# Kernel tuning notes

Hardware: AMD Instinct MI355X
Metric: run time of the kernel (lower is better)

Reference implementation:

```python
import jax, jax.numpy as jnp
import numpy as np

N = 50000
E = 800000
IN_DIM = 256
HID = 64
HEADS = 4
OUT_DIM = 40
NEG_SLOPE = 0.2


def _gatv2_conv(x, src, dst, Wl, bl, Wr, br, att, bias, concat):
    """PyG GATv2Conv (share_weights=False, eval mode, no attn dropout).
    src -> message source nodes, dst -> target nodes (softmax over dst)."""
    H, C = att.shape
    n = x.shape[0]
    xl = (x @ Wl + bl).reshape(n, H, C)  # source/message transform (lin_l)
    xr = (x @ Wr + br).reshape(n, H, C)  # target transform (lin_r)
    # per-edge logits: [E, H]
    s = xl[src] + xr[dst]                                  # [E,H,C]
    e = jnp.einsum('ehc,hc->eh', jax.nn.leaky_relu(s, NEG_SLOPE), att)
    # segment softmax over incoming edges of each target node
    m = jax.ops.segment_max(e, dst, num_segments=n)        # [N,H]
    m = jnp.where(jnp.isfinite(m), m, 0.0)                 # empty segments
    ex = jnp.exp(e - m[dst])
    denom = jax.ops.segment_sum(ex, dst, num_segments=n)   # [N,H]
    alpha = ex / (denom[dst] + 1e-16)                      # [E,H]
    out = jax.ops.segment_sum(alpha[:, :, None] * xl[src], dst, num_segments=n)
    if concat:
        out = out.reshape(n, H * C)
    else:
        out = out.mean(axis=1)
    return out + bias


def setup_inputs() -> dict:
    key = jax.random.key(0)
    ks = jax.random.split(key, 12)
    sc = 0.05
    return {
        'x': jax.random.normal(ks[0], (N, IN_DIM), jnp.float32),
        'src': jax.random.randint(ks[1], (E,), 0, N, jnp.int32),
        'dst': jax.random.randint(ks[2], (E,), 0, N, jnp.int32),
        'Wl1': jax.random.normal(ks[3], (IN_DIM, HEADS * HID), jnp.float32) * sc,
        'bl1': jnp.zeros((HEADS * HID,), jnp.float32),
        'Wr1': jax.random.normal(ks[4], (IN_DIM, HEADS * HID), jnp.float32) * sc,
        'br1': jnp.zeros((HEADS * HID,), jnp.float32),
        'att1': jax.random.normal(ks[5], (HEADS, HID), jnp.float32) * sc,
        'bias1': jnp.zeros((HEADS * HID,), jnp.float32),
        'Wl2': jax.random.normal(ks[6], (HEADS * HID, HEADS * HID), jnp.float32) * sc,
        'bl2': jnp.zeros((HEADS * HID,), jnp.float32),
        'Wr2': jax.random.normal(ks[7], (HEADS * HID, HEADS * HID), jnp.float32) * sc,
        'br2': jnp.zeros((HEADS * HID,), jnp.float32),
        'att2': jax.random.normal(ks[8], (HEADS, HID), jnp.float32) * sc,
        'bias2': jnp.zeros((HID,), jnp.float32),
        'Wc': jax.random.normal(ks[9], (HID, OUT_DIM), jnp.float32) * sc,
        'bc': jnp.zeros((OUT_DIM,), jnp.float32),
    }


def reference(x, src, dst, Wl1, bl1, Wr1, br1, att1, bias1,
              Wl2, bl2, Wr2, br2, att2, bias2, Wc, bc):
    h = _gatv2_conv(x, src, dst, Wl1, bl1, Wr1, br1, att1, bias1, concat=True)
    h = jax.nn.relu(h)  # dropout p applied only in training; eval -> identity
    h = _gatv2_conv(h, src, dst, Wl2, bl2, Wr2, br2, att2, bias2, concat=False)
    h = jax.nn.relu(h)
    return h @ Wc + bc  # [N, OUT_DIM]
```

## Files before the change

kernel.cpp:

```cpp
#include <hip/hip_runtime.h>
#include <hip/hip_bf16.h>
#include <math.h>


#define IN_DIM 256
#define HIDHC 256
#define HID 64
#define OUT_DIM 40

using half8  = __attribute__((ext_vector_type(8))) _Float16;
using half4  = __attribute__((ext_vector_type(4))) _Float16;
using half2v = __attribute__((ext_vector_type(2))) _Float16;
using f32x4  = __attribute__((ext_vector_type(4))) float;

__device__ __forceinline__ void gload16(const void* g, void* l) {
    __builtin_amdgcn_global_load_lds(
        (const __attribute__((address_space(1))) void*)g,
        (__attribute__((address_space(3))) void*)l, 16, 0, 0);
}

__global__ void hist_csr_prep(const int* __restrict__ src, const int* __restrict__ dst,
                              int* __restrict__ deg, int* __restrict__ csr,
                              int* __restrict__ oflow_cnt, int* __restrict__ oflow,
                              int E, int nbh,
                              const float* __restrict__ x, _Float16* __restrict__ Af,
                              const float* __restrict__ W0, const float* __restrict__ W1,
                              const float* __restrict__ W2, const float* __restrict__ W3,
                              _Float16* __restrict__ T, int n4, int nb_cvt) {
    int bid = blockIdx.x;
    if (bid < nbh) {
        int i = bid * 256 + threadIdx.x;
        if (i < E) {
            int d = dst[i];
            int r = atomicAdd(&deg[d], 1);
            if (r < 64) {
                csr[d * 64 + r] = src[i];
            } else {
                int q = atomicAdd(oflow_cnt, 1);
                oflow[2 * q] = d;
                oflow[2 * q + 1] = src[i];
            }
        }
    } else if (bid < nbh + nb_cvt) {
        int i = (bid - nbh) * 256 + threadIdx.x;
        if (i >= n4) return;
        float4 v = ((const float4*)x)[i];
        half4 h = { (_Float16)v.x, (_Float16)v.y, (_Float16)v.z, (_Float16)v.w };
        int node = i >> 6;
        int kb = (i & 63) * 4;
        size_t a = (size_t)(node >> 7) * 32768 + (size_t)(kb >> 3) * 1024
                 + (size_t)(node & 127) * 8 + (kb & 7);
        *(half4*)(Af + a) = h;
    } else {
        int widx = bid - nbh - nb_cvt;
        int wsel = widx >> 8, k = widx & 255, nn = threadIdx.x;
        const float* Wsel = (wsel == 0) ? W0 : (wsel == 1) ? W1
                          : (wsel == 2) ? W2 : W3;
        float v = Wsel[k * 256 + nn];
        size_t a = (size_t)wsel * 65536
                 + (size_t)(nn >> 7) * 32768 + (size_t)(k >> 5) * 4096
                 + (size_t)((k >> 3) & 3) * 1024 + (size_t)(nn & 127) * 8 + (k & 7);
        T[a] = (_Float16)v;
    }
}


__device__ __forceinline__ void gemm_tile(
    const _Float16* __restrict__ Apk,
    const _Float16* __restrict__ W0, const float* __restrict__ b0, _Float16* __restrict__ C0,
    const _Float16* __restrict__ W1, const float* __restrict__ b1, _Float16* __restrict__ C1,
    int M, int bx, int by, _Float16* sA, _Float16* sW)
{
    int tid = threadIdx.x;
    int bm = bx * 128;
    int bn = by * 128;

    int lane = tid & 63, w = tid >> 6;
    int z  = w >> 2, wq = w & 3;
    int r = lane & 15, q = lane >> 4;
    int m0 = (wq >> 1) * 64, n0 = (wq & 1) * 64;

    const _Float16* Abase = Apk + (size_t)bx * 32768;
    const _Float16* W0b   = W0  + (size_t)by * 32768;
    const _Float16* W1b   = W1  + (size_t)by * 32768;
    int go = tid * 8;

    f32x4 acc[4][4];
    #pragma unroll
    for (int i = 0; i < 4; ++i)
        #pragma unroll
        for (int j = 0; j < 4; ++j) acc[i][j] = (f32x4)0.f;

    gload16(Abase + go, sA + go);
    gload16(W0b + go, sW + go);
    gload16(W1b + go, sW + 4096 + go);
    __builtin_amdgcn_s_waitcnt(0);
    __syncthreads();

    #pragma unroll 1
    for (int kt = 0; kt < 8; ++kt) {
        int buf = kt & 1;
        if (kt < 7) {
            int k0 = (kt + 1) * 4096;
            gload16(Abase + k0 + go, sA + (buf ^ 1) * 4096 + go);
            gload16(W0b + k0 + go, sW + ((buf ^ 1) * 2 + 0) * 4096 + go);
            gload16(W1b + k0 + go, sW + ((buf ^ 1) * 2 + 1) * 4096 + go);
        }
        half8 a[4], b[4];
        #pragma unroll
        for (int i = 0; i < 4; ++i) {
            a[i] = *(const half8*)(sA + buf * 4096 + (q * 128 + m0 + i * 16 + r) * 8);
            b[i] = *(const half8*)(sW + (buf * 2 + z) * 4096 + (q * 128 + n0 + i * 16 + r) * 8);
        }
        #pragma unroll
        for (int i = 0; i < 4; ++i)
            #pragma unroll
            for (int j = 0; j < 4; ++j)
                acc[i][j] = __builtin_amdgcn_mfma_f32_16x16x32_f16(a[i], b[j], acc[i][j], 0, 0, 0);
        __builtin_amdgcn_s_waitcnt(0);
        __syncthreads();
    }

    const float* bias = z ? b1 : b0;
    _Float16*    C    = z ? C1 : C0;

    float bv[4];
    #pragma unroll
    for (int j = 0; j < 4; ++j) bv[j] = bias[bn + n0 + j * 16 + r];
    #pragma unroll
    for (int i = 0; i < 4; ++i) {
        #pragma unroll
        for (int reg = 0; reg < 4; ++reg) {
            int orow = bm + m0 + i * 16 + q * 4 + reg;
            if (orow < M) {
                #pragma unroll
                for (int j = 0; j < 4; ++j)
                    C[(size_t)orow * 256 + bn + n0 + j * 16 + r] =
                        (_Float16)(acc[i][j][reg] + bv[j]);
            }
        }
    }
}

__global__ __launch_bounds__(512) void gemm_dual(
    const _Float16* __restrict__ Apk,
    const _Float16* __restrict__ W0, const float* __restrict__ b0, _Float16* __restrict__ C0,
    const _Float16* __restrict__ W1, const float* __restrict__ b1, _Float16* __restrict__ C1,
    int M)
{
    __shared__ __align__(16) _Float16 sA[2 * 4096];
    __shared__ __align__(16) _Float16 sW[2 * 2 * 4096];
    gemm_tile(Apk, W0, b0, C0, W1, b1, C1, M, blockIdx.x, blockIdx.y, sA, sW);
}


__global__ __launch_bounds__(256) void gat_node(
    const _Float16* __restrict__ xl, const _Float16* __restrict__ xr,
    const float* __restrict__ att, const float* __restrict__ bias,
    const int* __restrict__ degv, const int* __restrict__ csr_src,
    const int* __restrict__ oflow_cnt, const int* __restrict__ oflow,
    void* __restrict__ out0, int n, int mode)
{
    int wid = threadIdx.x >> 6;
    int node = (blockIdx.x << 2) + wid;
    if (node >= n) return;
    int lane = threadIdx.x & 63;
    int H = lane >> 5;
    int p = lane & 31;

    const half2v c02 = { (_Float16)0.2f, (_Float16)0.2f };

    half8 xrh = *(const half8*)(xr + (size_t)node * HIDHC + p * 8);
    half2v xr01 = __builtin_shufflevector(xrh, xrh, 0, 1);
    half2v xr23 = __builtin_shufflevector(xrh, xrh, 2, 3);
    half2v xr45 = __builtin_shufflevector(xrh, xrh, 4, 5);
    half2v xr67 = __builtin_shufflevector(xrh, xrh, 6, 7);

    float4 af0 = *(const float4*)(att + p * 8);
    float4 af1 = *(const float4*)(att + p * 8 + 4);
    half2v at01 = { (_Float16)af0.x, (_Float16)af0.y };
    half2v at23 = { (_Float16)af0.z, (_Float16)af0.w };
    half2v at45 = { (_Float16)af1.x, (_Float16)af1.y };
    half2v at67 = { (_Float16)af1.z, (_Float16)af1.w };

    float acc[8];
    #pragma unroll
    for (int k = 0; k < 8; ++k) acc[k] = 0.f;
    float d = 0.f;

    auto edge_compute = [&](half8 h) {
        half2v h01 = __builtin_shufflevector(h, h, 0, 1);
        half2v h23 = __builtin_shufflevector(h, h, 2, 3);
        half2v h45 = __builtin_shufflevector(h, h, 4, 5);
        half2v h67 = __builtin_shufflevector(h, h, 6, 7);
        half2v s01 = h01 + xr01, s23 = h23 + xr23, s45 = h45 + xr45, s67 = h67 + xr67;
        half2v l01 = __builtin_elementwise_max(s01, s01 * c02);
        half2v l23 = __builtin_elementwise_max(s23, s23 * c02);
        half2v l45 = __builtin_elementwise_max(s45, s45 * c02);
        half2v l67 = __builtin_elementwise_max(s67, s67 * c02);
        float e = __builtin_amdgcn_fdot2(l01, at01, 0.f, false);
        e = __builtin_amdgcn_fdot2(l23, at23, e, false);
        e = __builtin_amdgcn_fdot2(l45, at45, e, false);
        e = __builtin_amdgcn_fdot2(l67, at67, e, false);
        e += __shfl_xor(e, 1);
        e += __shfl_xor(e, 2);
        e += __shfl_xor(e, 4);
        float pw = __expf(e);
        d += pw;
        #pragma unroll
        for (int k = 0; k < 8; ++k) acc[k] = fmaf(pw, (float)h[k], acc[k]);
    };
    auto edge_compute_single = [&](half8 h) {
        half2v h01 = __builtin_shufflevector(h, h, 0, 1);
        half2v h23 = __builtin_shufflevector(h, h, 2, 3);
        half2v h45 = __builtin_shufflevector(h, h, 4, 5);
        half2v h67 = __builtin_shufflevector(h, h, 6, 7);
        half2v s01 = h01 + xr01, s23 = h23 + xr23, s45 = h45 + xr45, s67 = h67 + xr67;
        half2v l01 = __builtin_elementwise_max(s01, s01 * c02);
        half2v l23 = __builtin_elementwise_max(s23, s23 * c02);
        half2v l45 = __builtin_elementwise_max(s45, s45 * c02);
        half2v l67 = __builtin_elementwise_max(s67, s67 * c02);
        float e = __builtin_amdgcn_fdot2(l01, at01, 0.f, false);
        e = __builtin_amdgcn_fdot2(l23, at23, e, false);
        e = __builtin_amdgcn_fdot2(l45, at45, e, false);
        e = __builtin_amdgcn_fdot2(l67, at67, e, false);
        e += __shfl_xor(e, 1);
        e += __shfl_xor(e, 2);
        e += __shfl_xor(e, 4);
        float pw = (H == 0) ? __expf(e) : 0.f;
        d += pw;
        #pragma unroll
        for (int k = 0; k < 8; ++k) acc[k] = fmaf(pw, (float)h[k], acc[k]);
    };

    int dg = __builtin_amdgcn_readfirstlane(degv[node]);
    int j0 = node << 6;

    int fast = min(dg, 64);
    int npf = fast >> 1;
    int idxv = 0;
    if (lane < fast) idxv = csr_src[j0 + lane];

    half8 hA, hB;
    if (npf > 0) { int s = __shfl(idxv, 0 + H, 64); hA = *(const half8*)(xl + (size_t)s * HIDHC + p * 8); }
    if (npf > 1) { int s = __shfl(idxv, 2 + H, 64); hB = *(const half8*)(xl + (size_t)s * HIDHC + p * 8); }
    int t = 0;
    for (; t + 4 <= npf; t += 2) {
        half8 ha = hA, hb = hB;
        { int s = __shfl(idxv, (t + 2) * 2 + H, 64); hA = *(const half8*)(xl + (size_t)s * HIDHC + p * 8); }
        { int s = __shfl(idxv, (t + 3) * 2 + H, 64); hB = *(const half8*)(xl + (size_t)s * HIDHC + p * 8); }
        edge_compute(ha);
        edge_compute(hb);
    }
    if (t + 2 <= npf) {
        half8 ha = hA, hb = hB;
        if (t + 2 < npf) { int s = __shfl(idxv, (t + 2) * 2 + H, 64); hA = *(const half8*)(xl + (size_t)s * HIDHC + p * 8); }
        edge_compute(ha);
        edge_compute(hb);
        t += 2;
    }
    if (t < npf) {
        edge_compute(hA);
    }
    if (fast & 1) {
        int s0 = __shfl(idxv, fast - 1, 64);
        half8 h = *(const half8*)(xl + (size_t)s0 * HIDHC + p * 8);
        edge_compute_single(h);
    }

    if (dg > 64) {
        int cnt = __builtin_amdgcn_readfirstlane(oflow_cnt[0]);
        for (int k = 0; k < cnt; ++k) {
            int dd = __builtin_amdgcn_readfirstlane(oflow[2 * k]);
            if (dd == node) {
                int ss = __builtin_amdgcn_readfirstlane(oflow[2 * k + 1]);
                half8 h = *(const half8*)(xl + (size_t)ss * HIDHC + p * 8);
                edge_compute_single(h);
            }
        }
    }

    d += __shfl_xor(d, 32);
    #pragma unroll
    for (int k = 0; k < 8; ++k) acc[k] += __shfl_xor(acc[k], 32);

    float inv = 1.f / (d + 1e-16f);
    float o[8];
    #pragma unroll
    for (int k = 0; k < 8; ++k) o[k] = acc[k] * inv;

    if (mode == 0) {
        if (H == 0) {
            float4 b0 = *(const float4*)(bias + p * 8);
            float4 b1 = *(const float4*)(bias + p * 8 + 4);
            float bb[8] = { b0.x, b0.y, b0.z, b0.w, b1.x, b1.y, b1.z, b1.w };
            half8 hh;
            #pragma unroll
            for (int k = 0; k < 8; ++k) hh[k] = (_Float16)fmaxf(o[k] + bb[k], 0.f);
            _Float16* dstp = (_Float16*)out0 + (size_t)(node >> 7) * 32768
                           + (size_t)p * 1024 + (size_t)(node & 127) * 8;
            *(half8*)dstp = hh;
        }
    } else {
        #pragma unroll
        for (int k = 0; k < 8; ++k) {
            o[k] += __shfl_xor(o[k], 8);
            o[k] += __shfl_xor(o[k], 16);
        }
        if (lane < 8) {
            float4 b0 = *(const float4*)(bias + p * 8);
            float4 b1 = *(const float4*)(bias + p * 8 + 4);
            float bb[8] = { b0.x, b0.y, b0.z, b0.w, b1.x, b1.y, b1.z, b1.w };
            float4 o0, o1;
            o0.x = fmaxf(o[0] * 0.25f + bb[0], 0.f);
            o0.y = fmaxf(o[1] * 0.25f + bb[1], 0.f);
            o0.z = fmaxf(o[2] * 0.25f + bb[2], 0.f);
            o0.w = fmaxf(o[3] * 0.25f + bb[3], 0.f);
            o1.x = fmaxf(o[4] * 0.25f + bb[4], 0.f);
            o1.y = fmaxf(o[5] * 0.25f + bb[5], 0.f);
            o1.z = fmaxf(o[6] * 0.25f + bb[6], 0.f);
            o1.w = fmaxf(o[7] * 0.25f + bb[7], 0.f);
            float* dstp = (float*)out0 + (size_t)node * HID + p * 8;
            *(float4*)dstp = o0;
            *(float4*)(dstp + 4) = o1;
        }
    }
}


__global__ __launch_bounds__(256) void final_linear(
    const float* __restrict__ h2, const float* __restrict__ Wc,
    const float* __restrict__ bc, float* __restrict__ out, int n)
{
    __shared__ float Ws[HID * OUT_DIM];
    __shared__ float bs[OUT_DIM];
    __shared__ float hs[64][HID + 1];

    for (int i = threadIdx.x; i < HID * OUT_DIM; i += 256) Ws[i] = Wc[i];
    if (threadIdx.x < OUT_DIM) bs[threadIdx.x] = bc[threadIdx.x];

    int n0 = blockIdx.x * 64;
    for (int i = threadIdx.x; i < 64 * HID; i += 256) {
        int r = i >> 6, c = i & 63;
        int node = n0 + r;
        hs[r][c] = (node < n) ? h2[(size_t)node * HID + c] : 0.f;
    }
    __syncthreads();

    for (int idx = threadIdx.x; idx < 64 * OUT_DIM; idx += 256) {
        int r = idx / OUT_DIM, o = idx % OUT_DIM;
        int node = n0 + r;
        if (node < n) {
            float s = bs[o];
            #pragma unroll
            for (int c = 0; c < HID; ++c) s = fmaf(hs[r][c], Ws[c * OUT_DIM + o], s);
            out[(size_t)node * OUT_DIM + o] = s;
        }
    }
}


extern "C" void kernel_launch(void* const* d_in, const int* in_sizes, int n_in,
                              void* d_out, int out_size, void* d_ws, size_t ws_size,
                              hipStream_t stream) {
    const int N = in_sizes[0] / IN_DIM;
    const int E = in_sizes[1];

    const float* x    = (const float*)d_in[0];
    const int*   src  = (const int*)d_in[1];
    const int*   dst  = (const int*)d_in[2];
    const float* Wl1  = (const float*)d_in[3];
    const float* bl1  = (const float*)d_in[4];
    const float* Wr1  = (const float*)d_in[5];
    const float* br1  = (const float*)d_in[6];
    const float* att1 = (const float*)d_in[7];
    const float* bias1= (const float*)d_in[8];
    const float* Wl2  = (const float*)d_in[9];
    const float* bl2  = (const float*)d_in[10];
    const float* Wr2  = (const float*)d_in[11];
    const float* br2  = (const float*)d_in[12];
    const float* att2 = (const float*)d_in[13];
    const float* bias2= (const float*)d_in[14];
    const float* Wc   = (const float*)d_in[15];
    const float* bc   = (const float*)d_in[16];

    char* ws = (char*)d_ws;
    size_t off = 0;
    const int NT = (N + 127) / 128;
    _Float16* xlh = (_Float16*)(ws + off); off += (size_t)N * HIDHC * 2;
    _Float16* xrh = (_Float16*)(ws + off); off += (size_t)N * HIDHC * 2;
    _Float16* Af  = (_Float16*)(ws + off); off += (size_t)NT * 32768 * 2;
    float*    h2  = (float*)(ws + off);    off += (size_t)N * HID * 4;
    _Float16* Wt  = (_Float16*)(ws + off); off += (size_t)4 * 65536 * 2;
    int* deg      = (int*)(ws + off); off += (size_t)N * 4;
    int* oflow_cnt= (int*)(ws + off); off += 4;
    int* csr      = (int*)(ws + off); off += (size_t)N * 64 * 4;
    int* oflow    = (int*)(ws + off); off += (size_t)E * 2 * 4;

    hipMemsetAsync(deg, 0, ((size_t)N + 1) * 4, stream);
    if (N & 127)
        hipMemsetAsync(Af + (size_t)(NT - 1) * 32768, 0, 32768 * 2, stream);

    const int nbh = (E + 255) / 256;
    const int n4 = N * HIDHC / 4;
    const int nb_cvt = (n4 + 255) / 256;
    hist_csr_prep<<<nbh + nb_cvt + 1024, 256, 0, stream>>>(
        src, dst, deg, csr, oflow_cnt, oflow, E, nbh,
        x, Af, Wl1, Wr1, Wl2, Wr2, Wt, n4, nb_cvt);

    const int KW = 65536;
    gemm_dual<<<dim3(NT, 2), 512, 0, stream>>>(Af,
        Wt + 0 * KW, bl1, xlh,
        Wt + 1 * KW, br1, xrh, N);
    gat_node<<<(N + 3) / 4, 256, 0, stream>>>(xlh, xrh, att1, bias1, deg, csr,
                                              oflow_cnt, oflow, (void*)Af, N, 0);
    gemm_dual<<<dim3(NT, 2), 512, 0, stream>>>(Af,
        Wt + 2 * KW, bl2, xlh,
        Wt + 3 * KW, br2, xrh, N);
    gat_node<<<(N + 3) / 4, 256, 0, stream>>>(xlh, xrh, att2, bias2, deg, csr,
                                              oflow_cnt, oflow, (void*)h2, N, 1);
    final_linear<<<(N + 63) / 64, 256, 0, stream>>>(h2, Wc, bc, (float*)d_out, N);
}
```

Baseline: 386.0 us.

## Split CSR build into rank histogram and scatter fused with first GEMM

The first kernel now only computes each edge's rank within its destination via atomics and stores it. The scatter of source indices into the CSR slots (plus overflow handling) moves into a new kernel that also runs the first dual GEMM, with scatter blocks placed ahead of the GEMM tiles. The aim is to overlap the memory-bound scatter with compute-bound GEMM work and shorten the atomic-heavy prep kernel. In exchange it adds an E-sized rank array that must be written and then read back.

```diff
diff --git a/kernel.cpp b/kernel.cpp
--- a/kernel.cpp
+++ b/kernel.cpp
@@ -19,28 +19,16 @@
         (__attribute__((address_space(3))) void*)l, 16, 0, 0);
 }
 
-__global__ void hist_csr_prep(const int* __restrict__ src, const int* __restrict__ dst,
-                              int* __restrict__ deg, int* __restrict__ csr,
-                              int* __restrict__ oflow_cnt, int* __restrict__ oflow,
-                              int E, int nbh,
-                              const float* __restrict__ x, _Float16* __restrict__ Af,
-                              const float* __restrict__ W0, const float* __restrict__ W1,
-                              const float* __restrict__ W2, const float* __restrict__ W3,
-                              _Float16* __restrict__ T, int n4, int nb_cvt) {
+__global__ void hist_prep(const int* __restrict__ dst, int* __restrict__ deg,
+                          int* __restrict__ rank, int E, int nbh,
+                          const float* __restrict__ x, _Float16* __restrict__ Af,
+                          const float* __restrict__ W0, const float* __restrict__ W1,
+                          const float* __restrict__ W2, const float* __restrict__ W3,
+                          _Float16* __restrict__ T, int n4, int nb_cvt) {
     int bid = blockIdx.x;
     if (bid < nbh) {
         int i = bid * 256 + threadIdx.x;
-        if (i < E) {
-            int d = dst[i];
-            int r = atomicAdd(&deg[d], 1);
-            if (r < 64) {
-                csr[d * 64 + r] = src[i];
-            } else {
-                int q = atomicAdd(oflow_cnt, 1);
-                oflow[2 * q] = d;
-                oflow[2 * q + 1] = src[i];
-            }
-        }
+        if (i < E) rank[i] = atomicAdd(&deg[dst[i]], 1);
     } else if (bid < nbh + nb_cvt) {
         int i = (bid - nbh) * 256 + threadIdx.x;
         if (i >= n4) return;
@@ -151,6 +139,36 @@
     __shared__ __align__(16) _Float16 sA[2 * 4096];
     __shared__ __align__(16) _Float16 sW[2 * 2 * 4096];
     gemm_tile(Apk, W0, b0, C0, W1, b1, C1, M, blockIdx.x, blockIdx.y, sA, sW);
+}
+
+__global__ __launch_bounds__(512) void gemm_scatter(
+    const _Float16* __restrict__ Apk,
+    const _Float16* __restrict__ W0, const float* __restrict__ b0, _Float16* __restrict__ C0,
+    const _Float16* __restrict__ W1, const float* __restrict__ b1, _Float16* __restrict__ C1,
+    int M, int nbs,
+    const int* __restrict__ src, const int* __restrict__ dst,
+    const int* __restrict__ rank, int* __restrict__ csr,
+    int* __restrict__ oflow_cnt, int* __restrict__ oflow, int E)
+{
+    __shared__ __align__(16) _Float16 sA[2 * 4096];
+    __shared__ __align__(16) _Float16 sW[2 * 2 * 4096];
+    if ((int)blockIdx.x < nbs) {
+        int e = blockIdx.x * 512 + threadIdx.x;
+        if (e < E) {
+            int r = rank[e];
+            int d = dst[e];
+            if (r < 64) {
+                csr[d * 64 + r] = src[e];
+            } else {
+                int q = atomicAdd(oflow_cnt, 1);
+                oflow[2 * q] = d;
+                oflow[2 * q + 1] = src[e];
+            }
+        }
+        return;
+    }
+    int g = blockIdx.x - nbs;
+    gemm_tile(Apk, W0, b0, C0, W1, b1, C1, M, g >> 1, g & 1, sA, sW);
 }
 
 
@@ -394,6 +412,7 @@
     _Float16* Wt  = (_Float16*)(ws + off); off += (size_t)4 * 65536 * 2;
     int* deg      = (int*)(ws + off); off += (size_t)N * 4;
     int* oflow_cnt= (int*)(ws + off); off += 4;
+    int* rank     = (int*)(ws + off); off += (size_t)E * 4;
     int* csr      = (int*)(ws + off); off += (size_t)N * 64 * 4;
     int* oflow    = (int*)(ws + off); off += (size_t)E * 2 * 4;
 
@@ -404,14 +423,16 @@
     const int nbh = (E + 255) / 256;
     const int n4 = N * HIDHC / 4;
     const int nb_cvt = (n4 + 255) / 256;
-    hist_csr_prep<<<nbh + nb_cvt + 1024, 256, 0, stream>>>(
-        src, dst, deg, csr, oflow_cnt, oflow, E, nbh,
-        x, Af, Wl1, Wr1, Wl2, Wr2, Wt, n4, nb_cvt);
+    hist_prep<<<nbh + nb_cvt + 1024, 256, 0, stream>>>(
+        dst, deg, rank, E, nbh, x, Af, Wl1, Wr1, Wl2, Wr2, Wt, n4, nb_cvt);
 
     const int KW = 65536;
-    gemm_dual<<<dim3(NT, 2), 512, 0, stream>>>(Af,
+    const int nbs = (E + 511) / 512;
+    gemm_scatter<<<nbs + 2 * NT, 512, 0, stream>>>(Af,
         Wt + 0 * KW, bl1, xlh,
-        Wt + 1 * KW, br1, xrh, N);
+        Wt + 1 * KW, br1, xrh, N, nbs,
+        src, dst, rank, csr, oflow_cnt, oflow, E);
+
     gat_node<<<(N + 3) / 4, 256, 0, stream>>>(xlh, xrh, att1, bias1, deg, csr,
                                               oflow_cnt, oflow, (void*)Af, N, 0);
     gemm_dual<<<dim3(NT, 2), 512, 0, stream>>>(Af,
```

New measurement: 387.9 us. No clear change (+0.5%).
